# Kernel tuning notes

Hardware: AMD Instinct MI355X
Metric: run time of the kernel (lower is better)

Reference implementation:

```python
import jax, jax.numpy as jnp
import numpy as np

TAU = 0.2
ALPHA = 0.8
LAM_POS = 1.5  # extrapolation lambda (hard positives)
EPS = 1e-8


def _cosine_sim(e):
    # torch F.cosine_similarity with eps=1e-8 norm clamping
    n = jnp.maximum(jnp.linalg.norm(e, axis=1), EPS)
    return (e @ e.T) / (n[:, None] * n[None, :])


def setup_inputs() -> dict:
    key = jax.random.key(0)
    N, D = 4096, 128
    emb = jax.random.normal(key, (N, D), dtype=jnp.float32)
    k = jnp.arange(N // 2, dtype=jnp.int32)
    i, j = 2 * k, 2 * k + 1
    # disjoint positive pairs, both orientations (matches symmetric set semantics)
    pp = jnp.concatenate([jnp.stack([i, j], 1), jnp.stack([j, i], 1)], 0)
    return {"embeddings": emb, "positive_pairs": pp, "stage_train": 1}


def reference(embeddings, positive_pairs, stage_train):
    N = embeddings.shape[0]
    pi, pj = positive_pairs[:, 0], positive_pairs[:, 1]
    Mp = jnp.zeros((N, N), dtype=bool).at[pi, pj].set(True)  # symmetric (both dirs in pairs)
    eye = jnp.eye(N, dtype=bool)
    Mn = (~eye) & (~Mp)  # negative pair mask

    # hard positive extrapolation: 1.5*e_i - 0.5*e_j (pairs disjoint -> order-free)
    hard_pos = jnp.zeros_like(embeddings).at[pi].set(
        LAM_POS * embeddings[pi] + (1.0 - LAM_POS) * embeddings[pj])

    # hard negative interpolation: loop over negatives in row-major order, last write
    idx = jnp.arange(N, dtype=jnp.int32)
    posmat = idx[:, None] * N + idx[None, :]          # enumeration position of pair (i,j)
    A = jnp.where(Mn, posmat, -1)
    col_max, col_arg = A.max(axis=0), A.argmax(axis=0)  # m as second element of (i,m)
    row_max, row_arg = A.max(axis=1), A.argmax(axis=1)  # m as first element of (m,j)
    partner = jnp.where(col_max > row_max, col_arg, row_arg)
    hard_neg = 0.5 * (embeddings + embeddings[partner])

    sim = _cosine_sim(embeddings)
    sim = jnp.where(Mp, _cosine_sim(hard_pos), jnp.where(Mn, _cosine_sim(hard_neg), sim))

    # contrastive loss with quantile hard mining
    mask = eye | Mp
    exp_sim = jnp.exp(sim / TAU)
    exp_masked = jnp.where(mask, 0.0, exp_sim)
    pos_ij = exp_sim[pi, pj]
    pos_ji = exp_sim[pj, pi]
    ei = exp_masked[pi]  # [2P, N]
    ej = exp_masked[pj]
    if stage_train:
        ti = jnp.quantile(ei, ALPHA, axis=1, keepdims=True)
        tj = jnp.quantile(ej, ALPHA, axis=1, keepdims=True)
        si = jnp.where(ei >= ti, ei, 0.0).sum(axis=1)
        sj = jnp.where(ej >= tj, ej, 0.0).sum(axis=1)
    else:
        si = ei.sum(axis=1)
        sj = ej.sum(axis=1)
    loss_ij = -jnp.log(pos_ij / (pos_ij + si))
    loss_ji = -jnp.log(pos_ji / (pos_ji + sj))
    num_pairs = positive_pairs.shape[0]
    return (loss_ij + loss_ji).sum() / (2 * num_pairs)
```

## Files before the change

kernel.cpp:

```cpp
#include <hip/hip_runtime.h>
#include <hip/hip_bf16.h>
#include <math.h>

#define D 128
#define INV_TAU 5.0f

typedef short bf16x8 __attribute__((ext_vector_type(8)));
typedef unsigned short u16x8 __attribute__((ext_vector_type(8)));
typedef float f32x4 __attribute__((ext_vector_type(4)));

__device__ __forceinline__ unsigned short bf16_bits(float v) {
    __hip_bfloat16 hb = __float2bfloat16(v);
    return *(unsigned short*)&hb;
}

__global__ void scatter_pos(const int* __restrict__ pp, int* __restrict__ pos,
                            float* __restrict__ out, int K) {
    int k = blockIdx.x * blockDim.x + threadIdx.x;
    if (k == 0) *out = 0.0f;
    if (k < K) pos[pp[2 * k]] = pp[2 * k + 1];
}

__global__ void prep_kernel(const float* __restrict__ emb, const int* __restrict__ pos,
                            const int* __restrict__ pp, unsigned short* __restrict__ hnn,
                            float* __restrict__ hpn, int N) {
    int b = blockIdx.x, d = threadIdx.x;
    __shared__ int sP;
    __shared__ float tmp[2];
    bool isHn = (b < N);
    if (isHn && d == 0) {
        int r = b, posr = pos[r];
        int jmax = -1;
        for (int j = N - 1; j >= 0; --j)
            if (j != r && j != posr) { jmax = j; break; }
        int imax = -1;
        for (int i = N - 1; i >= 0; --i)
            if (i != r && pos[i] != r) { imax = i; break; }
        long long rowm = (jmax >= 0) ? (long long)r * N + jmax : -1;
        long long colm = (imax >= 0) ? (long long)imax * N + r : -1;
        sP = (colm > rowm) ? (imax < 0 ? 0 : imax) : (jmax < 0 ? 0 : jmax);
    }
    __syncthreads();
    float h;
    int outrow;
    if (isHn) {
        int p = sP;
        h = 0.5f * (emb[b * D + d] + emb[p * D + d]);
        outrow = b;
    } else {
        int k = b - N;
        int a = pp[2 * k], bb = pp[2 * k + 1];
        h = 1.5f * emb[a * D + d] - 0.5f * emb[bb * D + d];
        outrow = a;
    }
    float ss = h * h;
#pragma unroll
    for (int off = 32; off > 0; off >>= 1) ss += __shfl_down(ss, off);
    if ((d & 63) == 0) tmp[d >> 6] = ss;
    __syncthreads();
    float inv = 1.0f / fmaxf(sqrtf(tmp[0] + tmp[1]), 1e-8f);
    if (isHn)
        hnn[outrow * D + d] = bf16_bits(h * inv);
    else
        hpn[outrow * D + d] = h * inv;
}

__global__ __launch_bounds__(256) void gemm_sim(const unsigned short* __restrict__ hnn,
                                                const int* __restrict__ pos,
                                                unsigned short* __restrict__ sims, int N) {
    __shared__ unsigned short As[128 * 136];
    __shared__ unsigned short Bs[128 * 136];
    __shared__ int pos_s[128];
    int tid = threadIdx.x;
    int rowBase = blockIdx.y * 128, colBase = blockIdx.x * 128;
    if (tid < 128) pos_s[tid] = pos[rowBase + tid];

    u16x8 ra[8], rb[8];
#pragma unroll
    for (int i = 0; i < 8; ++i) {
        int idx = i * 256 + tid;
        int row = idx >> 4, seg = idx & 15;
        ra[i] = *(const u16x8*)&hnn[(size_t)(rowBase + row) * D + seg * 8];
        rb[i] = *(const u16x8*)&hnn[(size_t)(colBase + row) * D + seg * 8];
    }
#pragma unroll
    for (int i = 0; i < 8; ++i) {
        int idx = i * 256 + tid;
        int row = idx >> 4, seg = idx & 15;
        *(u16x8*)&As[row * 136 + seg * 8] = ra[i];
        *(u16x8*)&Bs[row * 136 + seg * 8] = rb[i];
    }
    __syncthreads();

    int wave = tid >> 6, lane = tid & 63;
    int quad = lane >> 4, l15 = lane & 15;
    int rowhalf = wave >> 1, colhalf = wave & 1;

    f32x4 acc[4][4] = {};
#pragma unroll
    for (int kk = 0; kk < 4; ++kk) {
        bf16x8 af[4], bf[4];
#pragma unroll
        for (int rt = 0; rt < 4; ++rt)
            af[rt] = *(const bf16x8*)&As[(rowhalf * 64 + rt * 16 + l15) * 136 + kk * 32 + quad * 8];
#pragma unroll
        for (int ct = 0; ct < 4; ++ct)
            bf[ct] = *(const bf16x8*)&Bs[(colhalf * 64 + ct * 16 + l15) * 136 + kk * 32 + quad * 8];
#pragma unroll
        for (int rt = 0; rt < 4; ++rt)
#pragma unroll
            for (int ct = 0; ct < 4; ++ct)
                acc[rt][ct] = __builtin_amdgcn_mfma_f32_16x16x32_bf16(af[rt], bf[ct],
                                                                     acc[rt][ct], 0, 0, 0);
    }
    __syncthreads();

#pragma unroll
    for (int rt = 0; rt < 4; ++rt) {
#pragma unroll
        for (int rg = 0; rg < 4; ++rg) {
            int rloc = rowhalf * 64 + rt * 16 + quad * 4 + rg;
            int r = rowBase + rloc;
            int pr = pos_s[rloc];
#pragma unroll
            for (int ct = 0; ct < 4; ++ct) {
                int cloc = colhalf * 64 + ct * 16 + l15;
                int c = colBase + cloc;
                unsigned short u = bf16_bits(acc[rt][ct][rg]);
                unsigned short sv = (u & 0x8000u) ? (unsigned short)~u
                                                  : (unsigned short)(u | 0x8000u);
                if (c == r || c == pr) sv = 0x0080;
                As[rloc * 136 + cloc] = sv;
            }
        }
    }
    __syncthreads();

#pragma unroll
    for (int i = 0; i < 8; ++i) {
        int idx = i * 256 + tid;
        int row = idx >> 4, seg = idx & 15;
        *(u16x8*)&sims[(size_t)(rowBase + row) * N + colBase + seg * 8] =
            *(const u16x8*)&As[row * 136 + seg * 8];
    }
}

__global__ __launch_bounds__(512) void select_kernel(const unsigned short* __restrict__ sims,
                                                     const int* __restrict__ stage,
                                                     float* __restrict__ s_out, int N, int q) {
    int wave = threadIdx.x >> 6, lane = threadIdx.x & 63;
    int row = blockIdx.x * 8 + wave;
    const unsigned short* rp = sims + (size_t)row * N;

    unsigned s[64];
#pragma unroll
    for (int j = 0; j < 8; ++j) {
        u16x8 t = *(const u16x8*)&rp[j * 512 + lane * 8];
#pragma unroll
        for (int e = 0; e < 8; ++e) s[j * 8 + e] = (unsigned)(unsigned short)t[e];
    }

    unsigned T = 0;
    if (stage[0]) {
#pragma unroll
        for (int b = 15; b >= 0; --b) {
            unsigned cand = T | (1u << b);
            int cnt = 0;
#pragma unroll
            for (int i = 0; i < 64; ++i) cnt += (s[i] < cand);
#pragma unroll
            for (int off = 1; off < 64; off <<= 1) cnt += __shfl_xor(cnt, off);
            if (cnt <= q) T = cand;
        }
    }

    float sum = 0.0f;
#pragma unroll
    for (int i = 0; i < 64; ++i) {
        if (s[i] >= T) {
            unsigned raw = (s[i] & 0x8000u) ? (s[i] ^ 0x8000u) : (~s[i] & 0xFFFFu);
            sum += __expf(__uint_as_float(raw << 16) * INV_TAU);
        }
    }
#pragma unroll
    for (int off = 1; off < 64; off <<= 1) sum += __shfl_xor(sum, off);
    if (lane == 0) s_out[row] = sum;
}

__global__ __launch_bounds__(1024) void loss_kernel(const float* __restrict__ hpn,
                                                    const float* __restrict__ s,
                                                    const int* __restrict__ pp,
                                                    float* __restrict__ out, int K,
                                                    float scale) {
    int wave = threadIdx.x >> 6, lane = threadIdx.x & 63;
    int k = blockIdx.x * 16 + wave;
    float part = 0.0f;
    if (k < K) {
        int a = pp[2 * k], b = pp[2 * k + 1];
        float dsum = hpn[a * D + lane] * hpn[b * D + lane] +
                     hpn[a * D + lane + 64] * hpn[b * D + lane + 64];
#pragma unroll
        for (int off = 32; off > 0; off >>= 1) dsum += __shfl_down(dsum, off);
        if (lane == 0) {
            float p = __expf(dsum * INV_TAU);
            part = log1pf(s[a] / p) + log1pf(s[b] / p);
        }
    }
    __shared__ float red[16];
    if (lane == 0) red[wave] = part;
    __syncthreads();
    if (threadIdx.x == 0) {
        float tot = 0.0f;
#pragma unroll
        for (int w = 0; w < 16; ++w) tot += red[w];
        atomicAdd(out, tot * scale);
    }
}

extern "C" void kernel_launch(void* const* d_in, const int* in_sizes, int n_in,
                              void* d_out, int out_size, void* d_ws, size_t ws_size,
                              hipStream_t stream) {
    const float* emb = (const float*)d_in[0];
    const int* pp = (const int*)d_in[1];
    const int* stage = (const int*)d_in[2];
    int N = in_sizes[0] / D;
    int K = in_sizes[1] / 2;

    char* ws = (char*)d_ws;
    size_t offPos = 0;
    size_t offHnn = offPos + (size_t)N * 4;
    size_t offHpn = offHnn + (size_t)N * D * 2;
    size_t offS = offHpn + (size_t)N * D * 4;
    size_t offSims = offS + (size_t)N * 4;
    int* pos = (int*)(ws + offPos);
    unsigned short* hnn = (unsigned short*)(ws + offHnn);
    float* hpn = (float*)(ws + offHpn);
    float* s = (float*)(ws + offS);
    unsigned short* sims = (unsigned short*)(ws + offSims);

    scatter_pos<<<(K + 255) / 256, 256, 0, stream>>>(pp, pos, (float*)d_out, K);
    prep_kernel<<<N + K, D, 0, stream>>>(emb, pos, pp, hnn, hpn, N);
    dim3 g(N / 128, N / 128);
    gemm_sim<<<g, 256, 0, stream>>>(hnn, pos, sims, N);
    int q = (int)(0.8 * (double)(N - 1));
    select_kernel<<<N / 8, 512, 0, stream>>>(sims, stage, s, N, q);
    loss_kernel<<<(K + 15) / 16, 1024, 0, stream>>>(hpn, s, pp, (float*)d_out, K,
                                                    1.0f / (2.0f * K));
}
```

Baseline: 120.3 us.

## Exploit symmetry of similarity matrix: compute upper-triangle tiles and mirror

The similarity GEMM now launches only the upper-triangular 128x128 tiles. Each off-diagonal block writes both its tile and the transposed tile, using the B shared buffer as a transpose staging area and applying the column-side positive mask. This roughly halves the MFMA and load work. The global stores stay the same, and it adds a serial tile-index decode loop plus strided transposed shared-memory writes that may bank-conflict.

```diff
diff --git a/kernel.cpp b/kernel.cpp
--- a/kernel.cpp
+++ b/kernel.cpp
@@ -65,15 +65,21 @@
         hpn[outrow * D + d] = h * inv;
 }
 
-__global__ __launch_bounds__(256) void gemm_sim(const unsigned short* __restrict__ hnn,
-                                                const int* __restrict__ pos,
-                                                unsigned short* __restrict__ sims, int N) {
+__global__ __launch_bounds__(256) void gemm_sim_sym(const unsigned short* __restrict__ hnn,
+                                                    const int* __restrict__ pos,
+                                                    unsigned short* __restrict__ sims, int N) {
     __shared__ unsigned short As[128 * 136];
     __shared__ unsigned short Bs[128 * 136];
-    __shared__ int pos_s[128];
+    __shared__ int pos_r[128], pos_c[128];
     int tid = threadIdx.x;
-    int rowBase = blockIdx.y * 128, colBase = blockIdx.x * 128;
-    if (tid < 128) pos_s[tid] = pos[rowBase + tid];
+    int nT = N >> 7;
+    int t = blockIdx.x, trow = 0;
+    while (t >= nT - trow) { t -= nT - trow; ++trow; }
+    int tcol = trow + t;
+    int rowBase = trow * 128, colBase = tcol * 128;
+    bool diag = (trow == tcol);
+    if (tid < 128) pos_r[tid] = pos[rowBase + tid];
+    else pos_c[tid - 128] = pos[colBase + tid - 128];
 
     u16x8 ra[8], rb[8];
 #pragma unroll
@@ -121,7 +127,7 @@
         for (int rg = 0; rg < 4; ++rg) {
             int rloc = rowhalf * 64 + rt * 16 + quad * 4 + rg;
             int r = rowBase + rloc;
-            int pr = pos_s[rloc];
+            int pr = pos_r[rloc];
 #pragma unroll
             for (int ct = 0; ct < 4; ++ct) {
                 int cloc = colhalf * 64 + ct * 16 + l15;
@@ -129,8 +135,12 @@
                 unsigned short u = bf16_bits(acc[rt][ct][rg]);
                 unsigned short sv = (u & 0x8000u) ? (unsigned short)~u
                                                   : (unsigned short)(u | 0x8000u);
-                if (c == r || c == pr) sv = 0x0080;
-                As[rloc * 136 + cloc] = sv;
+                unsigned short svC = (c == r || c == pr) ? (unsigned short)0x0080 : sv;
+                As[rloc * 136 + cloc] = svC;
+                if (!diag) {
+                    unsigned short svT = (r == pos_c[cloc]) ? (unsigned short)0x0080 : sv;
+                    Bs[cloc * 136 + rloc] = svT;
+                }
             }
         }
     }
@@ -142,6 +152,15 @@
         int row = idx >> 4, seg = idx & 15;
         *(u16x8*)&sims[(size_t)(rowBase + row) * N + colBase + seg * 8] =
             *(const u16x8*)&As[row * 136 + seg * 8];
+    }
+    if (!diag) {
+#pragma unroll
+        for (int i = 0; i < 8; ++i) {
+            int idx = i * 256 + tid;
+            int row = idx >> 4, seg = idx & 15;
+            *(u16x8*)&sims[(size_t)(colBase + row) * N + rowBase + seg * 8] =
+                *(const u16x8*)&Bs[row * 136 + seg * 8];
+        }
     }
 }
 
@@ -237,11 +256,11 @@
     float* hpn = (float*)(ws + offHpn);
     float* s = (float*)(ws + offS);
     unsigned short* sims = (unsigned short*)(ws + offSims);
+    int nT = N >> 7;
 
     scatter_pos<<<(K + 255) / 256, 256, 0, stream>>>(pp, pos, (float*)d_out, K);
     prep_kernel<<<N + K, D, 0, stream>>>(emb, pos, pp, hnn, hpn, N);
-    dim3 g(N / 128, N / 128);
-    gemm_sim<<<g, 256, 0, stream>>>(hnn, pos, sims, N);
+    gemm_sim_sym<<<nT * (nT + 1) / 2, 256, 0, stream>>>(hnn, pos, sims, N);
     int q = (int)(0.8 * (double)(N - 1));
     select_kernel<<<N / 8, 512, 0, stream>>>(sims, stage, s, N, q);
     loss_kernel<<<(K + 15) / 16, 1024, 0, stream>>>(hpn, s, pp, (float*)d_out, K,
```

Result: slower. 125.5 us (+4.3%).
